# Performance work log

Hardware: AMD Instinct MI355X
Metric: run time of the kernel (lower is better)

Reference implementation:

```python
import jax, jax.numpy as jnp
import numpy as np

N_NODES = 100_000
N_EDGES = 1_000_000
D = 64


def setup_inputs() -> dict:
    key = jax.random.key(0)
    k1, k2, k3 = jax.random.split(key, 3)
    entity_embed = jax.random.normal(k1, (N_NODES, D), dtype=jnp.float32)
    # Guarantee every node has out-degree >= 1 (original uses 1/sqrt(out_degree)):
    # first N_NODES edges originate from each node once, rest are uniform random.
    src_extra = jax.random.randint(k2, (N_EDGES - N_NODES,), 0, N_NODES, dtype=jnp.int32)
    edge_src = jnp.concatenate([jnp.arange(N_NODES, dtype=jnp.int32), src_extra])
    edge_dst = jax.random.randint(k3, (N_EDGES,), 0, N_NODES, dtype=jnp.int32)
    return {"entity_embed": entity_embed, "edge_src": edge_src, "edge_dst": edge_dst}


def reference(entity_embed, edge_src, edge_dst):
    n = entity_embed.shape[0]
    # out-degree per node (used for BOTH src and dst normalization, as in the original)
    out_deg = jax.ops.segment_sum(
        jnp.ones_like(edge_src, dtype=entity_embed.dtype), edge_src, num_segments=n
    )
    sqrt_deg = 1.0 / jnp.sqrt(out_deg)  # [n]
    # message: src feature scaled by src degree norm  -> [n_edges, d]
    side = entity_embed[edge_src] * sqrt_deg[edge_src, None]
    # reduce: sum messages into destination mailbox    -> [n, d]
    agg = jax.ops.segment_sum(side, edge_dst, num_segments=n)
    # scale by dst degree norm
    return sqrt_deg[:, None] * agg
```

## Files before the change

### kernel.cpp

```cpp
#include <hip/hip_runtime.h>

#define DIM 64
#define TILE_B 9
#define TILE (1 << TILE_B)
#define CAPT 8192
#define CHUNK 2048
#define MAXNT 512

typedef unsigned int u32x4 __attribute__((ext_vector_type(4)));

__global__ void zero_gcur_kernel(int* __restrict__ g) {
    g[threadIdx.x + blockIdx.x * blockDim.x] = 0;
}

__global__ void partition_kernel(const int* __restrict__ src, const int* __restrict__ dst,
                                 int* __restrict__ gcur_d, int* __restrict__ gcur_s,
                                 unsigned int* __restrict__ ebuf,
                                 unsigned short* __restrict__ sbuf,
                                 int n_edges, int nt) {
    __shared__ int cnt_d[MAXNT];
    __shared__ int cnt_s[MAXNT];
    const int tid = threadIdx.x;
    for (int k = tid; k < nt; k += blockDim.x) { cnt_d[k] = 0; cnt_s[k] = 0; }
    __syncthreads();

    const int base = blockIdx.x * CHUNK;
    const int rem = min(CHUNK, n_edges - base);
    const int rem4 = rem >> 2;
    const int4* src4 = reinterpret_cast<const int4*>(src + base);
    const int4* dst4 = reinterpret_cast<const int4*>(dst + base);

    int4 sv[2], dv[2];
    bool ok[2];
    #pragma unroll
    for (int k = 0; k < 2; ++k) {
        int i4 = tid + k * 256;
        ok[k] = (i4 < rem4);
        if (ok[k]) { sv[k] = src4[i4]; dv[k] = dst4[i4]; }
    }
    #pragma unroll
    for (int k = 0; k < 2; ++k) {
        if (ok[k]) {
            atomicAdd(&cnt_d[dv[k].x >> TILE_B], 1); atomicAdd(&cnt_s[sv[k].x >> TILE_B], 1);
            atomicAdd(&cnt_d[dv[k].y >> TILE_B], 1); atomicAdd(&cnt_s[sv[k].y >> TILE_B], 1);
            atomicAdd(&cnt_d[dv[k].z >> TILE_B], 1); atomicAdd(&cnt_s[sv[k].z >> TILE_B], 1);
            atomicAdd(&cnt_d[dv[k].w >> TILE_B], 1); atomicAdd(&cnt_s[sv[k].w >> TILE_B], 1);
        }
    }
    if (tid == 0) {
        for (int j = rem & ~3; j < rem; ++j) {
            atomicAdd(&cnt_d[dst[base + j] >> TILE_B], 1);
            atomicAdd(&cnt_s[src[base + j] >> TILE_B], 1);
        }
    }
    __syncthreads();
    for (int k = tid; k < nt; k += blockDim.x) {
        int cd = cnt_d[k];
        if (cd) cnt_d[k] = atomicAdd(&gcur_d[k], cd);
        int cs = cnt_s[k];
        if (cs) cnt_s[k] = atomicAdd(&gcur_s[k], cs);
    }
    __syncthreads();
    #pragma unroll
    for (int k = 0; k < 2; ++k) {
        if (ok[k]) {
            int ss[4] = {sv[k].x, sv[k].y, sv[k].z, sv[k].w};
            int dd[4] = {dv[k].x, dv[k].y, dv[k].z, dv[k].w};
            #pragma unroll
            for (int q = 0; q < 4; ++q) {
                int s = ss[q], d = dd[q];
                int td = d >> TILE_B;
                int p = atomicAdd(&cnt_d[td], 1);
                if (p < CAPT)
                    ebuf[(size_t)td * CAPT + p] =
                        ((unsigned int)(d & (TILE - 1)) << 23) | (unsigned int)s;
                int ts = s >> TILE_B;
                int p2 = atomicAdd(&cnt_s[ts], 1);
                if (p2 < CAPT)
                    sbuf[(size_t)ts * CAPT + p2] = (unsigned short)(s & (TILE - 1));
            }
        }
    }
    if (tid == 0) {
        for (int j = rem & ~3; j < rem; ++j) {
            int s = src[base + j], d = dst[base + j];
            int td = d >> TILE_B;
            int p = atomicAdd(&cnt_d[td], 1);
            if (p < CAPT)
                ebuf[(size_t)td * CAPT + p] =
                    ((unsigned int)(d & (TILE - 1)) << 23) | (unsigned int)s;
            int ts = s >> TILE_B;
            int p2 = atomicAdd(&cnt_s[ts], 1);
            if (p2 < CAPT)
                sbuf[(size_t)ts * CAPT + p2] = (unsigned short)(s & (TILE - 1));
        }
    }
}

__global__ void tile_build_kernel(const unsigned int* __restrict__ ebuf,
                                  const unsigned short* __restrict__ sbuf,
                                  const int* __restrict__ gcur_d,
                                  const int* __restrict__ gcur_s,
                                  int* __restrict__ sorted_src,
                                  unsigned int* __restrict__ meta,
                                  float* __restrict__ sq, int n_nodes, int nt) {
    __shared__ unsigned int h[TILE];
    __shared__ int off[TILE];
    __shared__ int stmp[256];
    const int tid = threadIdx.x;

    if (blockIdx.x >= nt) {
        const int t = blockIdx.x - nt;
        for (int k = tid; k < TILE; k += blockDim.x) h[k] = 0u;
        __syncthreads();
        const int ne = min(gcur_s[t], CAPT);
        const unsigned short* p = sbuf + (size_t)t * CAPT;
        for (int j = tid; j < ne; j += blockDim.x) atomicAdd(&h[p[j]], 1u);
        __syncthreads();
        const int base = t << TILE_B;
        for (int k = tid; k < TILE; k += blockDim.x) {
            int node = base + k;
            if (node < n_nodes) sq[node] = rsqrtf((float)h[k]);
        }
        return;
    }

    const int t = blockIdx.x;
    for (int k = tid; k < TILE; k += blockDim.x) h[k] = 0u;
    __syncthreads();
    const int ne = min(gcur_d[t], CAPT);
    const unsigned int* p = ebuf + (size_t)t * CAPT;
    for (int j = tid; j < ne; j += blockDim.x) atomicAdd(&h[p[j] >> 23], 1u);
    __syncthreads();
    int v0 = (int)h[2 * tid];
    int v1 = (int)h[2 * tid + 1];
    int pair = v0 + v1;
    stmp[tid] = pair;
    __syncthreads();
    for (int o = 1; o < 256; o <<= 1) {
        int x = (tid >= o) ? stmp[tid - o] : 0;
        __syncthreads();
        stmp[tid] += x;
        __syncthreads();
    }
    int excl = stmp[tid] - pair;
    off[2 * tid] = excl;
    off[2 * tid + 1] = excl + v0;
    const int base = t << TILE_B;
    {
        int n0 = base + 2 * tid;
        if (n0 < n_nodes)
            meta[n0] = ((unsigned int)min(excl, CAPT - 1) << 13) |
                       (unsigned int)min(v0, CAPT - 1);
        int n1 = n0 + 1;
        if (n1 < n_nodes)
            meta[n1] = ((unsigned int)min(excl + v0, CAPT - 1) << 13) |
                       (unsigned int)min(v1, CAPT - 1);
    }
    __syncthreads();
    for (int k = tid; k < TILE; k += blockDim.x) h[k] = (unsigned int)off[k];
    __syncthreads();
    for (int j = tid; j < ne; j += blockDim.x) {
        unsigned int e = p[j];
        int dlo = (int)(e >> 23);
        int pos = (int)atomicAdd(&h[dlo], 1u);
        sorted_src[(size_t)t * CAPT + pos] = (int)(e & 0x7fffffu);
    }
}

__global__ void scale_bf16_kernel(const float* __restrict__ embed, const float* __restrict__ sq,
                                  unsigned short* __restrict__ table, int n8) {
    int i = blockIdx.x * blockDim.x + threadIdx.x;
    if (i >= n8) return;
    float s = sq[i >> 3];
    const float4* p = reinterpret_cast<const float4*>(embed) + (size_t)i * 2;
    float4 v0 = p[0], v1 = p[1];
    float vals[8] = {v0.x, v0.y, v0.z, v0.w, v1.x, v1.y, v1.z, v1.w};
    unsigned int w[4];
    #pragma unroll
    for (int k = 0; k < 4; ++k) {
        unsigned int lo = __float_as_uint(vals[2 * k] * s);
        unsigned int hi = __float_as_uint(vals[2 * k + 1] * s);
        lo += 0x7fffu + ((lo >> 16) & 1u);
        hi += 0x7fffu + ((hi >> 16) & 1u);
        w[k] = (lo >> 16) | (hi & 0xffff0000u);
    }
    uint4 o = {w[0], w[1], w[2], w[3]};
    reinterpret_cast<uint4*>(table)[i] = o;
}

__global__ void aggregate_csr_kernel(const unsigned short* __restrict__ table,
                                     const float* __restrict__ sq,
                                     const int* __restrict__ sorted_src,
                                     const unsigned int* __restrict__ meta,
                                     float* __restrict__ out, int n_nodes) {
    int gid = blockIdx.x * blockDim.x + threadIdx.x;
    int node = gid >> 6;
    if (node >= n_nodes) return;
    int lane = threadIdx.x & 63;
    int g = lane >> 3;
    int c = lane & 7;
    unsigned int m = meta[node];
    float sn = sq[node];
    int start = ((node >> TILE_B) * CAPT) + (int)(m >> 13);
    int cnt = (int)(m & 0x1fffu);
    float a0 = 0.f, a1 = 0.f, a2 = 0.f, a3 = 0.f, a4 = 0.f, a5 = 0.f, a6 = 0.f, a7 = 0.f;
    int k = g;
    for (; k + 8 < cnt; k += 16) {
        int s1 = sorted_src[start + k];
        int s2 = sorted_src[start + k + 8];
        u32x4 r1 = *reinterpret_cast<const u32x4*>(table + (size_t)s1 * DIM + c * 8);
        u32x4 r2 = *reinterpret_cast<const u32x4*>(table + (size_t)s2 * DIM + c * 8);
        a0 += __uint_as_float(r1.x << 16);         a0 += __uint_as_float(r2.x << 16);
        a1 += __uint_as_float(r1.x & 0xffff0000u); a1 += __uint_as_float(r2.x & 0xffff0000u);
        a2 += __uint_as_float(r1.y << 16);         a2 += __uint_as_float(r2.y << 16);
        a3 += __uint_as_float(r1.y & 0xffff0000u); a3 += __uint_as_float(r2.y & 0xffff0000u);
        a4 += __uint_as_float(r1.z << 16);         a4 += __uint_as_float(r2.z << 16);
        a5 += __uint_as_float(r1.z & 0xffff0000u); a5 += __uint_as_float(r2.z & 0xffff0000u);
        a6 += __uint_as_float(r1.w << 16);         a6 += __uint_as_float(r2.w << 16);
        a7 += __uint_as_float(r1.w & 0xffff0000u); a7 += __uint_as_float(r2.w & 0xffff0000u);
    }
    if (k < cnt) {
        int s1 = sorted_src[start + k];
        u32x4 r1 = *reinterpret_cast<const u32x4*>(table + (size_t)s1 * DIM + c * 8);
        a0 += __uint_as_float(r1.x << 16);
        a1 += __uint_as_float(r1.x & 0xffff0000u);
        a2 += __uint_as_float(r1.y << 16);
        a3 += __uint_as_float(r1.y & 0xffff0000u);
        a4 += __uint_as_float(r1.z << 16);
        a5 += __uint_as_float(r1.z & 0xffff0000u);
        a6 += __uint_as_float(r1.w << 16);
        a7 += __uint_as_float(r1.w & 0xffff0000u);
    }
    #pragma unroll
    for (int mm = 8; mm <= 32; mm <<= 1) {
        a0 += __shfl_xor(a0, mm, 64); a1 += __shfl_xor(a1, mm, 64);
        a2 += __shfl_xor(a2, mm, 64); a3 += __shfl_xor(a3, mm, 64);
        a4 += __shfl_xor(a4, mm, 64); a5 += __shfl_xor(a5, mm, 64);
        a6 += __shfl_xor(a6, mm, 64); a7 += __shfl_xor(a7, mm, 64);
    }
    if (g == 0) {
        float* o = out + (size_t)node * DIM + c * 8;
        float4 r0 = {a0 * sn, a1 * sn, a2 * sn, a3 * sn};
        float4 r1 = {a4 * sn, a5 * sn, a6 * sn, a7 * sn};
        *reinterpret_cast<float4*>(o) = r0;
        *reinterpret_cast<float4*>(o + 4) = r1;
    }
}

__global__ void sdeg_atomic_kernel(const int* __restrict__ src, int* __restrict__ sdeg,
                                   int n_edges) {
    int i = blockIdx.x * blockDim.x + threadIdx.x;
    if (i < n_edges) atomicAdd(&sdeg[src[i]], 1);
}
__global__ void sq_from_sdeg_kernel(const int* __restrict__ sdeg, float* __restrict__ sq, int n) {
    int i = blockIdx.x * blockDim.x + threadIdx.x;
    if (i < n) sq[i] = rsqrtf((float)sdeg[i]);
}
__global__ void build_ll_kernel(const int* __restrict__ src, const int* __restrict__ dst,
                                int* __restrict__ head, int2* __restrict__ list, int n_edges) {
    int i = blockIdx.x * blockDim.x + threadIdx.x;
    if (i >= n_edges) return;
    int s = src[i];
    int d = dst[i];
    int prev = atomicExch(&head[d], i);
    list[i] = make_int2(prev, s);
}
__global__ void aggregate_ll_f32_kernel(const float* __restrict__ embed,
                                        const float* __restrict__ sq,
                                        const int* __restrict__ head,
                                        const int2* __restrict__ list,
                                        float* __restrict__ out, int n_nodes) {
    int gid = blockIdx.x * blockDim.x + threadIdx.x;
    int node = gid >> 3;
    if (node >= n_nodes) return;
    int c = gid & 7;
    int cur = head[node];
    float4 A0 = {0.f, 0.f, 0.f, 0.f}, A1 = {0.f, 0.f, 0.f, 0.f};
    while (cur >= 0) {
        int2 v = list[cur];
        cur = v.x;
        int s = v.y;
        float sc = sq[s];
        const float4* row = reinterpret_cast<const float4*>(embed + (size_t)s * DIM + c * 8);
        float4 v0 = row[0], v1 = row[1];
        A0.x += v0.x * sc; A0.y += v0.y * sc; A0.z += v0.z * sc; A0.w += v0.w * sc;
        A1.x += v1.x * sc; A1.y += v1.y * sc; A1.z += v1.z * sc; A1.w += v1.w * sc;
    }
    float sn = sq[node];
    float4 r0 = {A0.x * sn, A0.y * sn, A0.z * sn, A0.w * sn};
    float4 r1 = {A1.x * sn, A1.y * sn, A1.z * sn, A1.w * sn};
    float4* o = reinterpret_cast<float4*>(out + (size_t)node * DIM + c * 8);
    o[0] = r0; o[1] = r1;
}

static inline size_t align16(size_t x) { return (x + 15) & ~(size_t)15; }

extern "C" void kernel_launch(void* const* d_in, const int* in_sizes, int n_in,
                              void* d_out, int out_size, void* d_ws, size_t ws_size,
                              hipStream_t stream) {
    const float* embed = (const float*)d_in[0];
    const int*   src   = (const int*)d_in[1];
    const int*   dst   = (const int*)d_in[2];
    float*       out   = (float*)d_out;

    const int n_nodes = in_sizes[0] / DIM;
    const int n_edges = in_sizes[1];
    const int nt = (n_nodes + TILE - 1) >> TILE_B;
    const int tb = 256;

    size_t o_gcur_d = 0;
    size_t o_gcur_s = o_gcur_d + (size_t)MAXNT * 4;
    size_t o_sq     = o_gcur_s + (size_t)MAXNT * 4;
    size_t o_meta   = align16(o_sq + (size_t)n_nodes * 4);
    size_t o_A      = align16(o_meta + (size_t)n_nodes * 4);
    size_t A_bytes  = (size_t)nt * CAPT * 4;
    size_t table_b  = (size_t)n_nodes * DIM * 2;
    if (table_b > A_bytes) A_bytes = table_b;
    size_t o_B      = align16(o_A + A_bytes);
    size_t o_C      = align16(o_B + (size_t)nt * CAPT * 2);
    size_t need     = o_C + (size_t)nt * CAPT * 4;

    const bool fast = (nt <= MAXNT) && (n_nodes <= (1 << 23)) && (ws_size >= need);

    if (fast) {
        char* ws = (char*)d_ws;
        int* gcur_d = (int*)(ws + o_gcur_d);
        int* gcur_s = (int*)(ws + o_gcur_s);
        float* sq   = (float*)(ws + o_sq);
        unsigned int* meta = (unsigned int*)(ws + o_meta);
        unsigned int*   ebuf  = (unsigned int*)(ws + o_A);
        unsigned short* table = (unsigned short*)(ws + o_A);
        unsigned short* sbuf  = (unsigned short*)(ws + o_B);
        int* sorted_src = (int*)(ws + o_C);

        zero_gcur_kernel<<<2 * MAXNT / 256, 256, 0, stream>>>(gcur_d);

        const int g1 = (n_edges + CHUNK - 1) / CHUNK;
        partition_kernel<<<g1, tb, 0, stream>>>(src, dst, gcur_d, gcur_s, ebuf, sbuf,
                                                n_edges, nt);
        tile_build_kernel<<<2 * nt, tb, 0, stream>>>(ebuf, sbuf, gcur_d, gcur_s,
                                                     sorted_src, meta, sq, n_nodes, nt);
        const int n8 = n_nodes * (DIM / 8);
        scale_bf16_kernel<<<(n8 + tb - 1) / tb, tb, 0, stream>>>(embed, sq, table, n8);
        const long long at = (long long)n_nodes * 64;
        aggregate_csr_kernel<<<(int)((at + tb - 1) / tb), tb, 0, stream>>>(
            table, sq, sorted_src, meta, out, n_nodes);
    } else {
        int*   head = (int*)d_ws;
        float* sq   = (float*)(head + n_nodes);
        int*   sdeg = (int*)(sq + n_nodes);
        int2*  list = (int2*)(sdeg + n_nodes);
        (void)hipMemsetAsync(head, 0xFF, (size_t)n_nodes * 4, stream);
        (void)hipMemsetAsync(sdeg, 0, (size_t)n_nodes * 4, stream);
        sdeg_atomic_kernel<<<(n_edges + tb - 1) / tb, tb, 0, stream>>>(src, sdeg, n_edges);
        sq_from_sdeg_kernel<<<(n_nodes + tb - 1) / tb, tb, 0, stream>>>(sdeg, sq, n_nodes);
        build_ll_kernel<<<(n_edges + tb - 1) / tb, tb, 0, stream>>>(src, dst, head,
                                                                    list, n_edges);
        const int at = n_nodes * 8;
        aggregate_ll_f32_kernel<<<(at + tb - 1) / tb, tb, 0, stream>>>(
            embed, sq, head, list, out, n_nodes);
    }
}
```

Before: 87.37 us.

## Fuse bf16 scaling into tile build and pad CSR segments for paired index loads

Removes the separate scale_bf16 kernel. The source-degree blocks of tile_build now write the scaled bf16 table themselves once they have computed each tile's rsqrt degree. The table therefore gets its own workspace region instead of aliasing ebuf. Per-node segments in sorted_src are padded to even offsets, so the aggregate loop can fetch two source indices with one int2 load per lane. This saves a kernel launch and an extra read of sq, but the table conversion now runs on only the nt source-tile blocks, which may give less parallelism for that step.

```diff
diff --git a/kernel.cpp b/kernel.cpp
--- a/kernel.cpp
+++ b/kernel.cpp
@@ -101,12 +101,16 @@
                                   const unsigned short* __restrict__ sbuf,
                                   const int* __restrict__ gcur_d,
                                   const int* __restrict__ gcur_s,
+                                  const float* __restrict__ embed,
                                   int* __restrict__ sorted_src,
                                   unsigned int* __restrict__ meta,
-                                  float* __restrict__ sq, int n_nodes, int nt) {
+                                  float* __restrict__ sq,
+                                  unsigned short* __restrict__ table,
+                                  int n_nodes, int nt) {
     __shared__ unsigned int h[TILE];
     __shared__ int off[TILE];
     __shared__ int stmp[256];
+    __shared__ float hsq[TILE];
     const int tid = threadIdx.x;
 
     if (blockIdx.x >= nt) {
@@ -120,7 +124,31 @@
         const int base = t << TILE_B;
         for (int k = tid; k < TILE; k += blockDim.x) {
             int node = base + k;
-            if (node < n_nodes) sq[node] = rsqrtf((float)h[k]);
+            float s = rsqrtf((float)h[k]);
+            hsq[k] = s;
+            if (node < n_nodes) sq[node] = s;
+        }
+        __syncthreads();
+        const int rows = min(TILE, n_nodes - base);
+        for (int u = tid; u < rows * 8; u += blockDim.x) {
+            int row = u >> 3;
+            int ch = u & 7;
+            float s = hsq[row];
+            const float4* pe =
+                reinterpret_cast<const float4*>(embed + (size_t)(base + row) * DIM + ch * 8);
+            float4 v0 = pe[0], v1 = pe[1];
+            float vals[8] = {v0.x, v0.y, v0.z, v0.w, v1.x, v1.y, v1.z, v1.w};
+            unsigned int w[4];
+            #pragma unroll
+            for (int k2 = 0; k2 < 4; ++k2) {
+                unsigned int lo = __float_as_uint(vals[2 * k2] * s);
+                unsigned int hi = __float_as_uint(vals[2 * k2 + 1] * s);
+                lo += 0x7fffu + ((lo >> 16) & 1u);
+                hi += 0x7fffu + ((hi >> 16) & 1u);
+                w[k2] = (lo >> 16) | (hi & 0xffff0000u);
+            }
+            uint4 o = {w[0], w[1], w[2], w[3]};
+            reinterpret_cast<uint4*>(table + (size_t)(base + row) * DIM + ch * 8)[0] = o;
         }
         return;
     }
@@ -134,7 +162,9 @@
     __syncthreads();
     int v0 = (int)h[2 * tid];
     int v1 = (int)h[2 * tid + 1];
-    int pair = v0 + v1;
+    int v0p = (v0 + 1) & ~1;
+    int v1p = (v1 + 1) & ~1;
+    int pair = v0p + v1p;
     stmp[tid] = pair;
     __syncthreads();
     for (int o = 1; o < 256; o <<= 1) {
@@ -145,7 +175,7 @@
     }
     int excl = stmp[tid] - pair;
     off[2 * tid] = excl;
-    off[2 * tid + 1] = excl + v0;
+    off[2 * tid + 1] = excl + v0p;
     const int base = t << TILE_B;
     {
         int n0 = base + 2 * tid;
@@ -154,7 +184,7 @@
                        (unsigned int)min(v0, CAPT - 1);
         int n1 = n0 + 1;
         if (n1 < n_nodes)
-            meta[n1] = ((unsigned int)min(excl + v0, CAPT - 1) << 13) |
+            meta[n1] = ((unsigned int)min(excl + v0p, CAPT - 1) << 13) |
                        (unsigned int)min(v1, CAPT - 1);
     }
     __syncthreads();
@@ -164,29 +194,9 @@
         unsigned int e = p[j];
         int dlo = (int)(e >> 23);
         int pos = (int)atomicAdd(&h[dlo], 1u);
-        sorted_src[(size_t)t * CAPT + pos] = (int)(e & 0x7fffffu);
-    }
-}
-
-__global__ void scale_bf16_kernel(const float* __restrict__ embed, const float* __restrict__ sq,
-                                  unsigned short* __restrict__ table, int n8) {
-    int i = blockIdx.x * blockDim.x + threadIdx.x;
-    if (i >= n8) return;
-    float s = sq[i >> 3];
-    const float4* p = reinterpret_cast<const float4*>(embed) + (size_t)i * 2;
-    float4 v0 = p[0], v1 = p[1];
-    float vals[8] = {v0.x, v0.y, v0.z, v0.w, v1.x, v1.y, v1.z, v1.w};
-    unsigned int w[4];
-    #pragma unroll
-    for (int k = 0; k < 4; ++k) {
-        unsigned int lo = __float_as_uint(vals[2 * k] * s);
-        unsigned int hi = __float_as_uint(vals[2 * k + 1] * s);
-        lo += 0x7fffu + ((lo >> 16) & 1u);
-        hi += 0x7fffu + ((hi >> 16) & 1u);
-        w[k] = (lo >> 16) | (hi & 0xffff0000u);
-    }
-    uint4 o = {w[0], w[1], w[2], w[3]};
-    reinterpret_cast<uint4*>(table)[i] = o;
+        if (pos < CAPT)
+            sorted_src[(size_t)t * CAPT + pos] = (int)(e & 0x7fffffu);
+    }
 }
 
 __global__ void aggregate_csr_kernel(const unsigned short* __restrict__ table,
@@ -205,24 +215,20 @@
     int start = ((node >> TILE_B) * CAPT) + (int)(m >> 13);
     int cnt = (int)(m & 0x1fffu);
     float a0 = 0.f, a1 = 0.f, a2 = 0.f, a3 = 0.f, a4 = 0.f, a5 = 0.f, a6 = 0.f, a7 = 0.f;
-    int k = g;
-    for (; k + 8 < cnt; k += 16) {
-        int s1 = sorted_src[start + k];
-        int s2 = sorted_src[start + k + 8];
-        u32x4 r1 = *reinterpret_cast<const u32x4*>(table + (size_t)s1 * DIM + c * 8);
-        u32x4 r2 = *reinterpret_cast<const u32x4*>(table + (size_t)s2 * DIM + c * 8);
-        a0 += __uint_as_float(r1.x << 16);         a0 += __uint_as_float(r2.x << 16);
-        a1 += __uint_as_float(r1.x & 0xffff0000u); a1 += __uint_as_float(r2.x & 0xffff0000u);
-        a2 += __uint_as_float(r1.y << 16);         a2 += __uint_as_float(r2.y << 16);
-        a3 += __uint_as_float(r1.y & 0xffff0000u); a3 += __uint_as_float(r2.y & 0xffff0000u);
-        a4 += __uint_as_float(r1.z << 16);         a4 += __uint_as_float(r2.z << 16);
-        a5 += __uint_as_float(r1.z & 0xffff0000u); a5 += __uint_as_float(r2.z & 0xffff0000u);
-        a6 += __uint_as_float(r1.w << 16);         a6 += __uint_as_float(r2.w << 16);
-        a7 += __uint_as_float(r1.w & 0xffff0000u); a7 += __uint_as_float(r2.w & 0xffff0000u);
-    }
-    if (k < cnt) {
-        int s1 = sorted_src[start + k];
-        u32x4 r1 = *reinterpret_cast<const u32x4*>(table + (size_t)s1 * DIM + c * 8);
+    for (int k2 = 2 * g; k2 < cnt; k2 += 16) {
+        int2 ss = *reinterpret_cast<const int2*>(sorted_src + start + k2);
+        u32x4 r1 = *reinterpret_cast<const u32x4*>(table + (size_t)ss.x * DIM + c * 8);
+        if (k2 + 1 < cnt) {
+            u32x4 r2 = *reinterpret_cast<const u32x4*>(table + (size_t)ss.y * DIM + c * 8);
+            a0 += __uint_as_float(r2.x << 16);
+            a1 += __uint_as_float(r2.x & 0xffff0000u);
+            a2 += __uint_as_float(r2.y << 16);
+            a3 += __uint_as_float(r2.y & 0xffff0000u);
+            a4 += __uint_as_float(r2.z << 16);
+            a5 += __uint_as_float(r2.z & 0xffff0000u);
+            a6 += __uint_as_float(r2.w << 16);
+            a7 += __uint_as_float(r2.w & 0xffff0000u);
+        }
         a0 += __uint_as_float(r1.x << 16);
         a1 += __uint_as_float(r1.x & 0xffff0000u);
         a2 += __uint_as_float(r1.y << 16);
@@ -313,13 +319,11 @@
     size_t o_gcur_s = o_gcur_d + (size_t)MAXNT * 4;
     size_t o_sq     = o_gcur_s + (size_t)MAXNT * 4;
     size_t o_meta   = align16(o_sq + (size_t)n_nodes * 4);
-    size_t o_A      = align16(o_meta + (size_t)n_nodes * 4);
-    size_t A_bytes  = (size_t)nt * CAPT * 4;
-    size_t table_b  = (size_t)n_nodes * DIM * 2;
-    if (table_b > A_bytes) A_bytes = table_b;
-    size_t o_B      = align16(o_A + A_bytes);
-    size_t o_C      = align16(o_B + (size_t)nt * CAPT * 2);
-    size_t need     = o_C + (size_t)nt * CAPT * 4;
+    size_t o_ebuf   = align16(o_meta + (size_t)n_nodes * 4);
+    size_t o_table  = align16(o_ebuf + (size_t)nt * CAPT * 4);
+    size_t o_sbuf   = align16(o_table + (size_t)n_nodes * DIM * 2);
+    size_t o_sorted = align16(o_sbuf + (size_t)nt * CAPT * 2);
+    size_t need     = o_sorted + (size_t)nt * CAPT * 4;
 
     const bool fast = (nt <= MAXNT) && (n_nodes <= (1 << 23)) && (ws_size >= need);
 
@@ -329,20 +333,19 @@
         int* gcur_s = (int*)(ws + o_gcur_s);
         float* sq   = (float*)(ws + o_sq);
         unsigned int* meta = (unsigned int*)(ws + o_meta);
-        unsigned int*   ebuf  = (unsigned int*)(ws + o_A);
-        unsigned short* table = (unsigned short*)(ws + o_A);
-        unsigned short* sbuf  = (unsigned short*)(ws + o_B);
-        int* sorted_src = (int*)(ws + o_C);
+        unsigned int*   ebuf  = (unsigned int*)(ws + o_ebuf);
+        unsigned short* table = (unsigned short*)(ws + o_table);
+        unsigned short* sbuf  = (unsigned short*)(ws + o_sbuf);
+        int* sorted_src = (int*)(ws + o_sorted);
 
         zero_gcur_kernel<<<2 * MAXNT / 256, 256, 0, stream>>>(gcur_d);
 
         const int g1 = (n_edges + CHUNK - 1) / CHUNK;
         partition_kernel<<<g1, tb, 0, stream>>>(src, dst, gcur_d, gcur_s, ebuf, sbuf,
                                                 n_edges, nt);
-        tile_build_kernel<<<2 * nt, tb, 0, stream>>>(ebuf, sbuf, gcur_d, gcur_s,
-                                                     sorted_src, meta, sq, n_nodes, nt);
-        const int n8 = n_nodes * (DIM / 8);
-        scale_bf16_kernel<<<(n8 + tb - 1) / tb, tb, 0, stream>>>(embed, sq, table, n8);
+        tile_build_kernel<<<2 * nt, tb, 0, stream>>>(ebuf, sbuf, gcur_d, gcur_s, embed,
+                                                     sorted_src, meta, sq, table,
+                                                     n_nodes, nt);
         const long long at = (long long)n_nodes * 64;
         aggregate_csr_kernel<<<(int)((at + tb - 1) / tb), tb, 0, stream>>>(
             table, sq, sorted_src, meta, out, n_nodes);
```

Result: faster. 83.06 us (-4.9%).
